# Performance work log

Hardware: AMD Instinct MI355X
Metric: run time of the kernel (lower is better)

## Reference

```python
import jax, jax.numpy as jnp
import numpy as np

N = 20000
NEG_SLOPE = 0.2


def gatv2_layer(x, src, dst, edge_attr, Wl, bl, Wr, br, We, att, bias, H, C):
    """PyG GATv2Conv: add self-loops (edge_attr fill='mean'), gather-score-softmax-aggregate."""
    n = x.shape[0]
    E = src.shape[0]
    # --- add self loops, self-loop edge_attr = mean of incoming edge_attr per node ---
    ea_sum = jax.ops.segment_sum(edge_attr, dst, num_segments=n)
    deg = jax.ops.segment_sum(jnp.ones((E, 1), x.dtype), dst, num_segments=n)
    ea_loop = ea_sum / jnp.maximum(deg, 1.0)
    loop = jnp.arange(n)
    src_a = jnp.concatenate([src, loop])
    dst_a = jnp.concatenate([dst, loop])
    ea = jnp.concatenate([edge_attr, ea_loop], axis=0)
    # --- linear projections ---
    xl = (x @ Wl + bl).reshape(n, H, C)   # source-side features
    xr = (x @ Wr + br).reshape(n, H, C)   # target-side features
    e = (ea @ We).reshape(-1, H, C)       # edge features
    # --- per-edge GATv2 attention score ---
    m = xl[src_a] + xr[dst_a] + e                          # [E', H, C]
    s = jnp.sum(jax.nn.leaky_relu(m, NEG_SLOPE) * att, -1)  # [E', H]
    # --- softmax over incoming edges of each target node ---
    smax = jax.ops.segment_max(s, dst_a, num_segments=n)
    ex = jnp.exp(s - smax[dst_a])
    denom = jax.ops.segment_sum(ex, dst_a, num_segments=n)
    alpha = ex / (denom[dst_a] + 1e-16)                    # [E', H]
    # --- aggregate messages (alpha * x_l[src]) ---
    out = jax.ops.segment_sum(alpha[..., None] * xl[src_a], dst_a, num_segments=n)
    return out.reshape(n, H * C) + bias


def setup_inputs() -> dict:
    key = jax.random.key(0)
    ks = jax.random.split(key, 20)
    F, HID, H1, A = 128, 32, 8, 128
    E = 640000
    d = {}
    d["x"] = jax.random.normal(ks[0], (N, F), jnp.float32)
    d["edge_index"] = jax.random.randint(ks[1], (2, E), 0, N, jnp.int32).astype(jnp.int64)
    d["edge_attr"] = jax.random.normal(ks[2], (E, 1), jnp.float32)
    # layer 1 params (in=F, out=HID, heads=H1)
    d["W1l"] = jax.random.normal(ks[3], (F, H1 * HID), jnp.float32) * 0.05
    d["b1l"] = jnp.zeros((H1 * HID,), jnp.float32)
    d["W1r"] = jax.random.normal(ks[4], (F, H1 * HID), jnp.float32) * 0.05
    d["b1r"] = jnp.zeros((H1 * HID,), jnp.float32)
    d["We1"] = jax.random.normal(ks[5], (1, H1 * HID), jnp.float32) * 0.05
    d["att1"] = jax.random.normal(ks[6], (H1, HID), jnp.float32) * 0.05
    d["bias1"] = jnp.zeros((H1 * HID,), jnp.float32)
    # layer 2 params (in=H1*HID, out=A, heads=1)
    d["W2l"] = jax.random.normal(ks[7], (H1 * HID, A), jnp.float32) * 0.05
    d["b2l"] = jnp.zeros((A,), jnp.float32)
    d["W2r"] = jax.random.normal(ks[8], (H1 * HID, A), jnp.float32) * 0.05
    d["b2r"] = jnp.zeros((A,), jnp.float32)
    d["We2"] = jax.random.normal(ks[9], (1, A), jnp.float32) * 0.05
    d["att2"] = jax.random.normal(ks[10], (1, A), jnp.float32) * 0.05
    d["bias2"] = jnp.zeros((A,), jnp.float32)
    d["alpha"] = jnp.array(0.0, jnp.float32)
    return d


def reference(x, edge_index, edge_attr, W1l, b1l, W1r, b1r, We1, att1, bias1,
              W2l, b2l, W2r, b2r, We2, att2, bias2, alpha):
    src, dst = edge_index[0], edge_index[1]
    h = jax.nn.relu(gatv2_layer(x, src, dst, edge_attr, W1l, b1l, W1r, b1r,
                                We1, att1, bias1, H=8, C=32))
    h = jax.nn.relu(gatv2_layer(h, src, dst, edge_attr, W2l, b2l, W2r, b2r,
                                We2, att2, bias2, H=1, C=128))
    pooled = jnp.mean(h, axis=0, keepdims=True)  # global_mean_pool, single graph -> [1, A]
    return jax.nn.softmax(pooled, axis=1), jax.nn.sigmoid(alpha)
```

## Files before the change

kernel.cpp:

```cpp
#include <hip/hip_runtime.h>
#include <math.h>

#define NEG_SLOPE 0.2f
#define LOG2E 1.4426950408889634f

typedef __attribute__((ext_vector_type(8))) short short8;
typedef __attribute__((ext_vector_type(4))) float f32x4;
typedef __attribute__((ext_vector_type(2))) float v2f;

__device__ __forceinline__ int imin(int a, int b) { return a < b ? a : b; }

__device__ __forceinline__ unsigned int f2bf(float f) {
    unsigned int u = __float_as_uint(f);
    return (u + 0x7fffu + ((u >> 16) & 1u)) >> 16;
}
__device__ __forceinline__ float fast_exp2(float x) {
#if __has_builtin(__builtin_amdgcn_exp2f)
    return __builtin_amdgcn_exp2f(x);
#else
    return exp2f(x);
#endif
}
__device__ __forceinline__ unsigned char f2fp8(float v) {
    return (unsigned char)(__builtin_amdgcn_cvt_pk_fp8_f32(v, v, 0, false) & 0xff);
}
template <int CTRL>
__device__ __forceinline__ float dpp_add(float v) {
    int t = __builtin_amdgcn_update_dpp(0, __float_as_int(v), CTRL, 0xF, 0xF, true);
    return v + __int_as_float(t);
}
__device__ __forceinline__ v2f pk_fma(v2f a, v2f b, v2f c) {
    v2f d;
    asm("v_pk_fma_f32 %0, %1, %2, %3" : "=v"(d) : "v"(a), "v"(b), "v"(c));
    return d;
}
__device__ __forceinline__ v2f pk_add(v2f a, v2f b) {
    v2f d;
    asm("v_pk_add_f32 %0, %1, %2" : "=v"(d) : "v"(a), "v"(b));
    return d;
}

__global__ void fused_prep(const int* __restrict__ ei, const float* __restrict__ ea,
                           unsigned long long* __restrict__ hist, int E,
                           const float* __restrict__ x, unsigned short* __restrict__ xb, int nF4,
                           const float* __restrict__ W1l, const float* __restrict__ W1r,
                           const float* __restrict__ W2l, const float* __restrict__ W2r,
                           const float* __restrict__ b1l, const float* __restrict__ b1r,
                           const float* __restrict__ b2l, const float* __restrict__ b2r,
                           unsigned short* __restrict__ Wt1, unsigned short* __restrict__ Wt2,
                           float* __restrict__ b1cat, float* __restrict__ b2cat,
                           int F, int HC1, int HC2) {
    int i = blockIdx.x * blockDim.x + threadIdx.x;
    if (i < E) {
        int d = ei[E + i];
        long long fx = (long long)__float2int_rn(ea[i] * 65536.0f);
        unsigned long long v = ((unsigned long long)fx << 32) | 1ull;
        atomicAdd(&hist[(size_t)d * 8], v);
        return;
    }
    int j = i - E;
    if (j < nF4) {
        float4 v = ((const float4*)x)[j];
        uint2 r;
        r.x = f2bf(v.x) | (f2bf(v.y) << 16);
        r.y = f2bf(v.z) | (f2bf(v.w) << 16);
        ((uint2*)xb)[j] = r;
        return;
    }
    int k = j - nF4;
    int S1 = F * HC1, S2 = HC1 * HC2;
    if (k < S1) {
        int kk = k / HC1, nn = k - kk * HC1;
        Wt1[(size_t)nn * F + kk] = (unsigned short)f2bf(W1l[k]);
    } else if (k < 2 * S1) {
        int m = k - S1;
        int kk = m / HC1, nn = m - kk * HC1;
        Wt1[(size_t)(HC1 + nn) * F + kk] = (unsigned short)f2bf(W1r[m]);
    } else if (k < 2 * S1 + S2) {
        int m = k - 2 * S1;
        int kk = m / HC2, nn = m - kk * HC2;
        Wt2[(size_t)nn * HC1 + kk] = (unsigned short)f2bf(W2l[m]);
    } else if (k < 2 * S1 + 2 * S2) {
        int m = k - 2 * S1 - S2;
        int kk = m / HC2, nn = m - kk * HC2;
        Wt2[(size_t)(HC2 + nn) * HC1 + kk] = (unsigned short)f2bf(W2r[m]);
    } else if (k < 2 * S1 + 2 * S2 + 2 * HC1) {
        int m = k - 2 * S1 - 2 * S2;
        b1cat[m] = (m < HC1) ? b1l[m] : b1r[m - HC1];
    } else if (k < 2 * S1 + 2 * S2 + 2 * HC1 + 2 * HC2) {
        int m = k - 2 * S1 - 2 * S2 - 2 * HC1;
        b2cat[m] = (m < HC2) ? b2l[m] : b2r[m - HC2];
    }
}

__global__ void scan_a(const unsigned long long* __restrict__ hist, int* __restrict__ bsum, int n) {
    __shared__ int wred[4];
    int base = blockIdx.x * 1024;
    int tid = threadIdx.x;
    int s = 0;
#pragma unroll
    for (int k = 0; k < 4; ++k) {
        int i = base + tid + k * 256;
        if (i < n) s += (int)(hist[(size_t)i * 8] & 0xffffffffull);
    }
#pragma unroll
    for (int off = 32; off > 0; off >>= 1) s += __shfl_xor(s, off, 64);
    if ((tid & 63) == 0) wred[tid >> 6] = s;
    __syncthreads();
    if (tid == 0) bsum[blockIdx.x] = wred[0] + wred[1] + wred[2] + wred[3];
}

__global__ void scan_c(const unsigned long long* __restrict__ hist,
                       const int* __restrict__ bsum, int* __restrict__ row_ptr,
                       int* __restrict__ wptr_pad, float* __restrict__ ea_loop,
                       int n, int B) {
    __shared__ int wtot[4];
    __shared__ int sh_base;
    int tid = threadIdx.x;
    int wid = tid >> 6, lane = tid & 63;
    int i0 = blockIdx.x * 1024 + tid * 4;
    int dcnt[4]; float esum[4];
#pragma unroll
    for (int k = 0; k < 4; ++k) {
        if (i0 + k < n) {
            unsigned long long h = hist[(size_t)(i0 + k) * 8];
            dcnt[k] = (int)(h & 0xffffffffull);
            esum[k] = (float)((int)(h >> 32)) * (1.0f / 65536.0f);
        } else { dcnt[k] = 0; esum[k] = 0.0f; }
    }
    int tsum = dcnt[0] + dcnt[1] + dcnt[2] + dcnt[3];
    int s = tsum;
#pragma unroll
    for (int off = 1; off < 64; off <<= 1) {
        int t = __shfl_up(s, off, 64);
        if (lane >= off) s += t;
    }
    if (lane == 63) wtot[wid] = s;
    if (tid < 64) {
        int v   = (tid < B) ? bsum[tid] : 0;
        int pre = (tid < (int)blockIdx.x) ? v : 0;
        int tot = v;
#pragma unroll
        for (int off = 32; off > 0; off >>= 1) {
            pre += __shfl_xor(pre, off, 64);
            tot += __shfl_xor(tot, off, 64);
        }
        if (tid == 0) {
            sh_base = pre;
            if (blockIdx.x == 0) row_ptr[n] = tot;
        }
    }
    __syncthreads();
    int wpre = 0;
#pragma unroll
    for (int k = 0; k < 4; ++k) if (k < wid) wpre += wtot[k];
    int pre = sh_base + wpre + (s - tsum);
    if (i0 < n) {
        int4 e;
        e.x = pre;
        e.y = pre + dcnt[0];
        e.z = e.y + dcnt[1];
        e.w = e.z + dcnt[2];
        *(int4*)(row_ptr + i0) = e;
        int ev[4] = { e.x, e.y, e.z, e.w };
        float4 el;
        el.x = esum[0] / fmaxf((float)dcnt[0], 1.0f);
        el.y = esum[1] / fmaxf((float)dcnt[1], 1.0f);
        el.z = esum[2] / fmaxf((float)dcnt[2], 1.0f);
        el.w = esum[3] / fmaxf((float)dcnt[3], 1.0f);
        *(float4*)(ea_loop + i0) = el;
#pragma unroll
        for (int k = 0; k < 4; ++k) wptr_pad[(size_t)(i0 + k) * 16] = ev[k];
    }
}

__global__ void edge_scatter(const int* __restrict__ ei, const float* __restrict__ ea,
                             int* __restrict__ wptr_pad, int2* __restrict__ spk, int E) {
    int e = blockIdx.x * blockDim.x + threadIdx.x;
    if (e < E) {
        int d = ei[E + e];
        int pos = atomicAdd(&wptr_pad[(size_t)d * 16], 1);
        spk[pos] = make_int2(ei[e], __float_as_int(ea[e]));
    }
}

template <bool OUT_FP8>
__global__ void __launch_bounds__(256)
gemm_bf16(const unsigned short* __restrict__ A, const unsigned short* __restrict__ Bt,
          const float* __restrict__ bias, void* __restrict__ Cv,
          int M, int N, int K) {
    __shared__ __attribute__((aligned(16))) unsigned short As[64 * 40];
    __shared__ __attribute__((aligned(16))) unsigned short Bs[64 * 40];
    int tid  = threadIdx.x;
    int wave = tid >> 6, lane = tid & 63;
    int m0 = blockIdx.x * 64, n0 = blockIdx.y * 64;
    int row = tid >> 2, kg = (tid & 3) * 8;

    f32x4 acc[4] = {};
    for (int kk = 0; kk < K; kk += 32) {
        int gm = m0 + row;
        uint4 av;
        if (gm < M) av = *(const uint4*)(A + (size_t)gm * K + kk + kg);
        else        av = make_uint4(0, 0, 0, 0);
        *(uint4*)&As[row * 40 + kg] = av;
        uint4 bv = *(const uint4*)(Bt + (size_t)(n0 + row) * K + kk + kg);
        *(uint4*)&Bs[row * 40 + kg] = bv;
        __syncthreads();
        short8 a = *(const short8*)&As[(wave * 16 + (lane & 15)) * 40 + (lane >> 4) * 8];
#pragma unroll
        for (int g = 0; g < 4; ++g) {
            short8 b = *(const short8*)&Bs[(g * 16 + (lane & 15)) * 40 + (lane >> 4) * 8];
            acc[g] = __builtin_amdgcn_mfma_f32_16x16x32_bf16(a, b, acc[g], 0, 0, 0);
        }
        __syncthreads();
    }
#pragma unroll
    for (int g = 0; g < 4; ++g) {
        int col = n0 + g * 16 + (lane & 15);
        float bs = bias[col];
#pragma unroll
        for (int r = 0; r < 4; ++r) {
            int grow = m0 + wave * 16 + (lane >> 4) * 4 + r;
            if (grow < M) {
                float val = acc[g][r] + bs;
                if constexpr (OUT_FP8) {
                    ((unsigned char*)Cv)[(size_t)grow * N + col] = f2fp8(val);
                } else {
                    ((unsigned short*)Cv)[(size_t)grow * N + col] = (unsigned short)f2bf(val);
                }
            }
        }
    }
}

template <int NG>
__device__ __forceinline__ void unp2(uint2 u, v2f* xf) {
    xf[0] = __builtin_amdgcn_cvt_pk_f32_fp8(u.x, false);
    xf[1] = __builtin_amdgcn_cvt_pk_f32_fp8(u.x, true);
    if constexpr (NG == 4) {
        xf[2] = __builtin_amdgcn_cvt_pk_f32_fp8(u.y, false);
        xf[3] = __builtin_amdgcn_cvt_pk_f32_fp8(u.y, true);
    }
}
template <int G>
__device__ __forceinline__ float grp_reduce32(float vs) {
    vs = dpp_add<0xB1>(vs);
    if constexpr (G >= 4)  vs = dpp_add<0x4E>(vs);
    if constexpr (G >= 8)  vs = dpp_add<0x141>(vs);
    if constexpr (G >= 16) vs = dpp_add<0x140>(vs);
    if constexpr (G >= 32) {
        int t = __builtin_amdgcn_ds_swizzle(__float_as_int(vs), 0x401F);
        vs += __int_as_float(t);
    }
    return vs;
}

template <int HC, int STRIDE, int C, int OUT_MODE>
__global__ void __launch_bounds__(256)
gat_agg(const unsigned char* __restrict__ xlr,
        const float* __restrict__ We, const float* __restrict__ att,
        const float* __restrict__ bias,
        const int* __restrict__ row_ptr, const int2* __restrict__ spk,
        const float* __restrict__ ea_loop,
        void* __restrict__ out, int n) {
    constexpr int NV = HC / 32;
    constexpr int NG = NV / 2;
    constexpr int G  = C / NV;
    constexpr int SHIFT = (STRIDE == 512) ? 9 : 8;
    constexpr float K23 = 2.0f / 3.0f;
    __shared__ float red[4][128];
    int wave = threadIdx.x >> 6;
    int lane = threadIdx.x & 63;
    int node = blockIdx.x * 4 + wave;
    bool active = node < n;
    if (OUT_MODE == 0 && !active) return;
    unsigned int lo32 = (unsigned int)(lane & 31) * NV;
    int half = lane >> 5;

    float vout[NV];
#pragma unroll
    for (int j = 0; j < NV; ++j) vout[j] = 0.0f;

    if (active) {
        auto ldd = [&](unsigned int off) -> uint2 {
            uint2 r;
            if constexpr (NV == 8) r = *(const uint2*)(xlr + off);
            else { r.x = *(const unsigned int*)(xlr + off); r.y = 0u; }
            return r;
        };
        auto gat = [&](int s) -> uint2 {
            return ldd(((unsigned int)s << SHIFT) + lo32);
        };

        v2f xr2[NG], We2[NG], att62[NG], o2[NG];
        unp2<NG>(ldd(((unsigned int)node << SHIFT) + HC + lo32), xr2);
#pragma unroll
        for (int g = 0; g < NG; ++g) {
            We2[g]   = *(const v2f*)(We  + lo32 + 2 * g);
            v2f a    = *(const v2f*)(att + lo32 + 2 * g);
            att62[g] = a * (0.6f * LOG2E);
            o2[g]    = v2f{0.0f, 0.0f};
        }
        float l = 0.0f;

        int start = __builtin_amdgcn_readfirstlane(row_ptr[node]);
        int end   = __builtin_amdgcn_readfirstlane(row_ptr[node + 1]);
        float ea_l = ea_loop[node];

        auto process = [&](uint2 du, float w, bool maskhi) {
            v2f xf[NG];
            unp2<NG>(du, xf);
            v2f w2 = {w, w};
            v2f vs6 = {0.0f, 0.0f};
            float vs4 = 0.0f;
#pragma unroll
            for (int g = 0; g < NG; ++g) {
                v2f t  = pk_fma(w2, We2[g], xr2[g]);
                v2f mm = pk_add(xf[g], t);
                vs6 = pk_fma(att62[g], mm, vs6);
                vs4 = fmaf(fabsf(mm.x), att62[g].x, vs4);
                vs4 = fmaf(fabsf(mm.y), att62[g].y, vs4);
            }
            float vs = fmaf(K23, vs4, vs6.x + vs6.y);
            vs = grp_reduce32<G>(vs);
            float pr = fast_exp2(vs);
            if (maskhi && lane >= 32) pr = 0.0f;
            l += pr;
            v2f pr2 = {pr, pr};
#pragma unroll
            for (int g = 0; g < NG; ++g) o2[g] = pk_fma(xf[g], pr2, o2[g]);
        };
        auto W = [&](int2 s) -> float { return __int_as_float(s.y); };

        process(ldd(((unsigned int)node << SHIFT) + lo32), ea_l, true);

        int cnt = end - start;
        int npair = cnt >> 1;
        const int2* pp = spk + start + half;

        if (npair >= 8) {
            int2 s0 = pp[0],  s1 = pp[2],  s2 = pp[4],  s3 = pp[6];
            int2 s4 = pp[8],  s5 = pp[10], s6 = pp[12], s7 = pp[14];
            uint2 g0 = gat(s0.x), g1 = gat(s1.x), g2 = gat(s2.x), g3 = gat(s3.x);
            int p = 0;
            for (; p + 16 <= npair; p += 8) {
                uint2 h0 = gat(s4.x), h1 = gat(s5.x), h2 = gat(s6.x), h3 = gat(s7.x);
                float w0 = W(s0), w1 = W(s1), w2 = W(s2), w3 = W(s3);
                s0 = pp[2*(p+8)];  s1 = pp[2*(p+9)];
                s2 = pp[2*(p+10)]; s3 = pp[2*(p+11)];
                process(g0, w0, false); process(g1, w1, false);
                process(g2, w2, false); process(g3, w3, false);
                g0 = gat(s0.x); g1 = gat(s1.x); g2 = gat(s2.x); g3 = gat(s3.x);
                float w4 = W(s4), w5 = W(s5), w6 = W(s6), w7 = W(s7);
                s4 = pp[2*(p+12)]; s5 = pp[2*(p+13)];
                s6 = pp[2*(p+14)]; s7 = pp[2*(p+15)];
                process(h0, w4, false); process(h1, w5, false);
                process(h2, w6, false); process(h3, w7, false);
            }
            uint2 h0 = gat(s4.x), h1 = gat(s5.x), h2 = gat(s6.x), h3 = gat(s7.x);
            process(g0, W(s0), false); process(g1, W(s1), false);
            process(g2, W(s2), false); process(g3, W(s3), false);
            process(h0, W(s4), false); process(h1, W(s5), false);
            process(h2, W(s6), false); process(h3, W(s7), false);
            for (int k = p + 8; k < npair; ++k) {
                int2 t = pp[2 * k];
                process(gat(t.x), W(t), false);
            }
        } else {
            for (int k = 0; k < npair; ++k) {
                int2 t = pp[2 * k];
                process(gat(t.x), W(t), false);
            }
        }
        if (cnt & 1) {
            int2 st = spk[end - 1];
            process(gat(st.x), W(st), true);
        }

        l += __shfl_xor(l, 32, 64);
#pragma unroll
        for (int g = 0; g < NG; ++g) {
            o2[g].x += __shfl_xor(o2[g].x, 32, 64);
            o2[g].y += __shfl_xor(o2[g].y, 32, 64);
        }
        float inv = 1.0f / (l + 1e-16f);

        if (lane < 32) {
#pragma unroll
            for (int g = 0; g < NG; ++g) {
                v2f b = *(const v2f*)(bias + lo32 + 2 * g);
                vout[2 * g]     = fmaxf(o2[g].x * inv + b.x, 0.0f);
                vout[2 * g + 1] = fmaxf(o2[g].y * inv + b.y, 0.0f);
            }
            if constexpr (OUT_MODE == 0) {
                unsigned short* op = (unsigned short*)out + (size_t)node * HC + lo32;
                if constexpr (NV == 8) {
                    uint4 t;
                    t.x = f2bf(vout[0]) | (f2bf(vout[1]) << 16);
                    t.y = f2bf(vout[2]) | (f2bf(vout[3]) << 16);
                    t.z = f2bf(vout[4]) | (f2bf(vout[5]) << 16);
                    t.w = f2bf(vout[6]) | (f2bf(vout[7]) << 16);
                    *(uint4*)op = t;
                } else {
                    uint2 t;
                    t.x = f2bf(vout[0]) | (f2bf(vout[1]) << 16);
                    t.y = f2bf(vout[2]) | (f2bf(vout[3]) << 16);
                    *(uint2*)op = t;
                }
            }
        }
    }

    if constexpr (OUT_MODE == 1) {
        if (lane < 32) {
#pragma unroll
            for (int j = 0; j < NV; ++j) red[wave][lo32 + j] = vout[j];
        }
        __syncthreads();
        if (wave == 0) {
            int c = lane;
            float a = red[0][c] + red[1][c] + red[2][c] + red[3][c];
            float b = red[0][c + 64] + red[1][c + 64] + red[2][c + 64] + red[3][c + 64];
            float* pacc = (float*)out + (size_t)(blockIdx.x & 255) * 128;
            atomicAdd(&pacc[c], a);
            atomicAdd(&pacc[c + 64], b);
        }
    }
}

__global__ void __launch_bounds__(1024)
pool_final(const float* __restrict__ partial, int nb,
           const float* __restrict__ alpha_in,
           float* __restrict__ out, int n) {
    __shared__ float acc[8][128];
    __shared__ float red[4];
    int t = threadIdx.x & 127;
    int g = threadIdx.x >> 7;
    float s = 0.0f;
    for (int b = g; b < nb; b += 8) s += partial[b * 128 + t];
    acc[g][t] = s;
    __syncthreads();
    if (threadIdx.x < 128) {
        float tot = 0.0f;
#pragma unroll
        for (int k = 0; k < 8; ++k) tot += acc[k][t];
        float mean = tot / (float)n;
        float mx = mean;
#pragma unroll
        for (int off = 32; off > 0; off >>= 1) mx = fmaxf(mx, __shfl_xor(mx, off, 64));
        if ((t & 63) == 0) red[t >> 6] = mx;
        __syncthreads();
        mx = fmaxf(red[0], red[1]);
        float ex = __expf(mean - mx);
        float sm = ex;
#pragma unroll
        for (int off = 32; off > 0; off >>= 1) sm += __shfl_xor(sm, off, 64);
        if ((t & 63) == 0) red[2 + (t >> 6)] = sm;
        __syncthreads();
        sm = red[2] + red[3];
        out[t] = ex / sm;
        if (t == 0) out[128] = 1.0f / (1.0f + __expf(-alpha_in[0]));
    }
}

extern "C" void kernel_launch(void* const* d_in, const int* in_sizes, int n_in,
                              void* d_out, int out_size, void* d_ws, size_t ws_size,
                              hipStream_t stream) {
    const float* x    = (const float*)d_in[0];
    const int*   ei   = (const int*)d_in[1];
    const float* ea   = (const float*)d_in[2];
    const float* W1l  = (const float*)d_in[3];
    const float* b1l  = (const float*)d_in[4];
    const float* W1r  = (const float*)d_in[5];
    const float* b1r  = (const float*)d_in[6];
    const float* We1  = (const float*)d_in[7];
    const float* att1 = (const float*)d_in[8];
    const float* bias1= (const float*)d_in[9];
    const float* W2l  = (const float*)d_in[10];
    const float* b2l  = (const float*)d_in[11];
    const float* W2r  = (const float*)d_in[12];
    const float* b2r  = (const float*)d_in[13];
    const float* We2  = (const float*)d_in[14];
    const float* att2 = (const float*)d_in[15];
    const float* bias2= (const float*)d_in[16];
    const float* alpha= (const float*)d_in[17];
    float* out = (float*)d_out;

    const int F = 128, HC1 = 256, HC2 = 128;
    const int n = in_sizes[0] / F;
    const int E = in_sizes[1] / 2;
    const int B = (n + 1023) / 1024;

    char* ws = (char*)d_ws;
    size_t off = 0;
    auto alloc = [&](size_t bytes) { size_t p = off; off += (bytes + 255) & ~(size_t)255; return p; };

    unsigned long long* hist = (unsigned long long*)(ws + alloc((size_t)n * 8 * 8));
    int*   row_ptr = (int*)  (ws + alloc((size_t)(n + 1) * 4));
    int*   wptr    = (int*)  (ws + alloc((size_t)n * 16 * 4));
    float* ea_loop = (float*)(ws + alloc((size_t)n * 4));
    int*   bsum    = (int*)  (ws + alloc(64 * 4));
    int2*  spk     = (int2*) (ws + alloc((size_t)E * 8));
    unsigned short* xb   = (unsigned short*)(ws + alloc((size_t)n * F * 2));
    unsigned short* Wt1  = (unsigned short*)(ws + alloc((size_t)F * (2 * HC1) * 2));
    unsigned short* Wt2  = (unsigned short*)(ws + alloc((size_t)HC1 * (2 * HC2) * 2));
    float* b1cat   = (float*)(ws + alloc((size_t)2 * HC1 * 4));
    float* b2cat   = (float*)(ws + alloc((size_t)2 * HC2 * 4));
    unsigned char* xlr1 = (unsigned char*)(ws + alloc((size_t)n * 2 * HC1));
    unsigned short* h1  = (unsigned short*)(ws + alloc((size_t)n * HC1 * 2));
    float* partial = (float*)(ws + alloc((size_t)256 * 128 * 4));
    unsigned char* xlr2 = xlr1;
    const int NB_SLOTS = 256;

    (void)hipMemsetAsync(hist, 0, (size_t)n * 8 * 8, stream);
    (void)hipMemsetAsync(partial, 0, (size_t)NB_SLOTS * 128 * 4, stream);

    int tb = 256;
    {
        int nF4  = n * F / 4;
        int WTOT = 2 * F * HC1 + 2 * HC1 * HC2 + 2 * HC1 + 2 * HC2;
        int total = E + nF4 + WTOT;
        fused_prep<<<(total + tb - 1) / tb, tb, 0, stream>>>(
            ei, ea, hist, E, x, xb, nF4,
            W1l, W1r, W2l, W2r, b1l, b1r, b2l, b2r,
            Wt1, Wt2, b1cat, b2cat, F, HC1, HC2);
    }
    scan_a<<<B, 256, 0, stream>>>(hist, bsum, n);
    scan_c<<<B, 256, 0, stream>>>(hist, bsum, row_ptr, wptr, ea_loop, n, B);
    edge_scatter<<<(E + tb - 1) / tb, tb, 0, stream>>>(ei, ea, wptr, spk, E);

    {
        dim3 grid((n + 63) / 64, (2 * HC1) / 64);
        gemm_bf16<true><<<grid, 256, 0, stream>>>(xb, Wt1, b1cat, xlr1, n, 2 * HC1, F);
    }
    gat_agg<256, 512, 32, 0><<<(n + 3) / 4, 256, 0, stream>>>(
        xlr1, We1, att1, bias1, row_ptr, spk, ea_loop, h1, n);

    {
        dim3 grid((n + 63) / 64, (2 * HC2) / 64);
        gemm_bf16<true><<<grid, 256, 0, stream>>>(h1, Wt2, b2cat, xlr2, n, 2 * HC2, HC1);
    }
    gat_agg<128, 256, 128, 1><<<(n + 3) / 4, 256, 0, stream>>>(
        xlr2, We2, att2, bias2, row_ptr, spk, ea_loop, partial, n);

    pool_final<<<1, 1024, 0, stream>>>(partial, NB_SLOTS, alpha, out, n);
}
```

Measured before the change: 279.1 us.

## Split each node's edge list across two waves and merge via shared memory

The GAT aggregation kernel now gives each destination node two waves instead of one. Each wave processes half of the edge pairs, and the partial softmax numerators and denominators are combined through shared memory behind a block barrier. The deep 8-way gather prefetch pipeline is replaced with a shallower 2-deep one. This doubles the grid and aims to raise memory-level parallelism per node, at the cost of an extra __syncthreads, shared-memory traffic and fewer loads in flight per wave.

New measurement: 273.9 us. About the same (-1.9%).

```diff
diff --git a/kernel.cpp b/kernel.cpp
--- a/kernel.cpp
+++ b/kernel.cpp
@@ -268,44 +268,49 @@
     constexpr int G  = C / NV;
     constexpr int SHIFT = (STRIDE == 512) ? 9 : 8;
     constexpr float K23 = 2.0f / 3.0f;
-    __shared__ float red[4][128];
+    __shared__ float lsh[2][32];
+    __shared__ float osh[2][HC];
+    __shared__ float red[2][128];
     int wave = threadIdx.x >> 6;
     int lane = threadIdx.x & 63;
-    int node = blockIdx.x * 4 + wave;
+    int nib  = wave >> 1;
+    int sub  = wave & 1;
+    int node = blockIdx.x * 2 + nib;
     bool active = node < n;
-    if (OUT_MODE == 0 && !active) return;
     unsigned int lo32 = (unsigned int)(lane & 31) * NV;
     int half = lane >> 5;
 
-    float vout[NV];
-#pragma unroll
-    for (int j = 0; j < NV; ++j) vout[j] = 0.0f;
+    v2f o2[NG];
+#pragma unroll
+    for (int g = 0; g < NG; ++g) o2[g] = v2f{0.0f, 0.0f};
+    float l = 0.0f;
+
+    v2f xr2[NG], We2[NG], att62[NG];
+
+    auto ldd = [&](unsigned int off) -> uint2 {
+        uint2 r;
+        if constexpr (NV == 8) r = *(const uint2*)(xlr + off);
+        else { r.x = *(const unsigned int*)(xlr + off); r.y = 0u; }
+        return r;
+    };
+    auto gat = [&](int s) -> uint2 {
+        return ldd(((unsigned int)s << SHIFT) + lo32);
+    };
+    auto W = [&](int2 s) -> float { return __int_as_float(s.y); };
 
     if (active) {
-        auto ldd = [&](unsigned int off) -> uint2 {
-            uint2 r;
-            if constexpr (NV == 8) r = *(const uint2*)(xlr + off);
-            else { r.x = *(const unsigned int*)(xlr + off); r.y = 0u; }
-            return r;
-        };
-        auto gat = [&](int s) -> uint2 {
-            return ldd(((unsigned int)s << SHIFT) + lo32);
-        };
-
-        v2f xr2[NG], We2[NG], att62[NG], o2[NG];
         unp2<NG>(ldd(((unsigned int)node << SHIFT) + HC + lo32), xr2);
 #pragma unroll
         for (int g = 0; g < NG; ++g) {
             We2[g]   = *(const v2f*)(We  + lo32 + 2 * g);
             v2f a    = *(const v2f*)(att + lo32 + 2 * g);
             att62[g] = a * (0.6f * LOG2E);
-            o2[g]    = v2f{0.0f, 0.0f};
-        }
-        float l = 0.0f;
+        }
 
         int start = __builtin_amdgcn_readfirstlane(row_ptr[node]);
         int end   = __builtin_amdgcn_readfirstlane(row_ptr[node + 1]);
-        float ea_l = ea_loop[node];
+        int cnt = end - start;
+        int npair = cnt >> 1;
 
         auto process = [&](uint2 du, float w, bool maskhi) {
             v2f xf[NG];
@@ -330,49 +335,41 @@
 #pragma unroll
             for (int g = 0; g < NG; ++g) o2[g] = pk_fma(xf[g], pr2, o2[g]);
         };
-        auto W = [&](int2 s) -> float { return __int_as_float(s.y); };
-
-        process(ldd(((unsigned int)node << SHIFT) + lo32), ea_l, true);
-
-        int cnt = end - start;
-        int npair = cnt >> 1;
-        const int2* pp = spk + start + half;
-
-        if (npair >= 8) {
-            int2 s0 = pp[0],  s1 = pp[2],  s2 = pp[4],  s3 = pp[6];
-            int2 s4 = pp[8],  s5 = pp[10], s6 = pp[12], s7 = pp[14];
-            uint2 g0 = gat(s0.x), g1 = gat(s1.x), g2 = gat(s2.x), g3 = gat(s3.x);
+
+        int lo = sub ? (npair >> 1) : 0;
+        int hi = sub ? npair : (npair >> 1);
+        int m = hi - lo;
+
+        if (sub == 0) {
+            float ea_l = ea_loop[node];
+            process(ldd(((unsigned int)node << SHIFT) + lo32), ea_l, true);
+        }
+
+        const int2* q = spk + start + half + 2 * lo;
+        if (m >= 2) {
+            int2 sA = q[0], sB = q[2];
+            uint2 gA = gat(sA.x);
             int p = 0;
-            for (; p + 16 <= npair; p += 8) {
-                uint2 h0 = gat(s4.x), h1 = gat(s5.x), h2 = gat(s6.x), h3 = gat(s7.x);
-                float w0 = W(s0), w1 = W(s1), w2 = W(s2), w3 = W(s3);
-                s0 = pp[2*(p+8)];  s1 = pp[2*(p+9)];
-                s2 = pp[2*(p+10)]; s3 = pp[2*(p+11)];
-                process(g0, w0, false); process(g1, w1, false);
-                process(g2, w2, false); process(g3, w3, false);
-                g0 = gat(s0.x); g1 = gat(s1.x); g2 = gat(s2.x); g3 = gat(s3.x);
-                float w4 = W(s4), w5 = W(s5), w6 = W(s6), w7 = W(s7);
-                s4 = pp[2*(p+12)]; s5 = pp[2*(p+13)];
-                s6 = pp[2*(p+14)]; s7 = pp[2*(p+15)];
-                process(h0, w4, false); process(h1, w5, false);
-                process(h2, w6, false); process(h3, w7, false);
+            for (; p + 4 <= m; p += 2) {
+                uint2 gB = gat(sB.x);
+                int2 sC = q[2 * (p + 2)], sD = q[2 * (p + 3)];
+                process(gA, W(sA), false);
+                uint2 gC = gat(sC.x);
+                process(gB, W(sB), false);
+                sA = sC; sB = sD; gA = gC;
             }
-            uint2 h0 = gat(s4.x), h1 = gat(s5.x), h2 = gat(s6.x), h3 = gat(s7.x);
-            process(g0, W(s0), false); process(g1, W(s1), false);
-            process(g2, W(s2), false); process(g3, W(s3), false);
-            process(h0, W(s4), false); process(h1, W(s5), false);
-            process(h2, W(s6), false); process(h3, W(s7), false);
-            for (int k = p + 8; k < npair; ++k) {
-                int2 t = pp[2 * k];
+            uint2 gB = gat(sB.x);
+            process(gA, W(sA), false);
+            process(gB, W(sB), false);
+            if (m - p == 3) {
+                int2 t = q[2 * (p + 2)];
                 process(gat(t.x), W(t), false);
             }
-        } else {
-            for (int k = 0; k < npair; ++k) {
-                int2 t = pp[2 * k];
-                process(gat(t.x), W(t), false);
-            }
-        }
-        if (cnt & 1) {
+        } else if (m == 1) {
+            int2 t = q[0];
+            process(gat(t.x), W(t), false);
+        }
+        if (sub == 1 && (cnt & 1)) {
             int2 st = spk[end - 1];
             process(gat(st.x), W(st), true);
         }
@@ -383,44 +380,61 @@
             o2[g].x += __shfl_xor(o2[g].x, 32, 64);
             o2[g].y += __shfl_xor(o2[g].y, 32, 64);
         }
+    }
+
+    if (sub == 1 && lane < 32) {
+        lsh[nib][lane] = l;
+#pragma unroll
+        for (int g = 0; g < NG; ++g) *(v2f*)&osh[nib][lo32 + 2 * g] = o2[g];
+    }
+    __syncthreads();
+
+    float vout[NV];
+#pragma unroll
+    for (int j = 0; j < NV; ++j) vout[j] = 0.0f;
+
+    if (sub == 0 && active && lane < 32) {
+        l += lsh[nib][lane];
+#pragma unroll
+        for (int g = 0; g < NG; ++g) {
+            v2f t = *(const v2f*)&osh[nib][lo32 + 2 * g];
+            o2[g] = pk_add(o2[g], t);
+        }
         float inv = 1.0f / (l + 1e-16f);
-
-        if (lane < 32) {
-#pragma unroll
-            for (int g = 0; g < NG; ++g) {
-                v2f b = *(const v2f*)(bias + lo32 + 2 * g);
-                vout[2 * g]     = fmaxf(o2[g].x * inv + b.x, 0.0f);
-                vout[2 * g + 1] = fmaxf(o2[g].y * inv + b.y, 0.0f);
+#pragma unroll
+        for (int g = 0; g < NG; ++g) {
+            v2f b = *(const v2f*)(bias + lo32 + 2 * g);
+            vout[2 * g]     = fmaxf(o2[g].x * inv + b.x, 0.0f);
+            vout[2 * g + 1] = fmaxf(o2[g].y * inv + b.y, 0.0f);
+        }
+        if constexpr (OUT_MODE == 0) {
+            unsigned short* op = (unsigned short*)out + (size_t)node * HC + lo32;
+            if constexpr (NV == 8) {
+                uint4 t;
+                t.x = f2bf(vout[0]) | (f2bf(vout[1]) << 16);
+                t.y = f2bf(vout[2]) | (f2bf(vout[3]) << 16);
+                t.z = f2bf(vout[4]) | (f2bf(vout[5]) << 16);
+                t.w = f2bf(vout[6]) | (f2bf(vout[7]) << 16);
+                *(uint4*)op = t;
+            } else {
+                uint2 t;
+                t.x = f2bf(vout[0]) | (f2bf(vout[1]) << 16);
+                t.y = f2bf(vout[2]) | (f2bf(vout[3]) << 16);
+                *(uint2*)op = t;
             }
-            if constexpr (OUT_MODE == 0) {
-                unsigned short* op = (unsigned short*)out + (size_t)node * HC + lo32;
-                if constexpr (NV == 8) {
-                    uint4 t;
-                    t.x = f2bf(vout[0]) | (f2bf(vout[1]) << 16);
-                    t.y = f2bf(vout[2]) | (f2bf(vout[3]) << 16);
-                    t.z = f2bf(vout[4]) | (f2bf(vout[5]) << 16);
-                    t.w = f2bf(vout[6]) | (f2bf(vout[7]) << 16);
-                    *(uint4*)op = t;
-                } else {
-                    uint2 t;
-                    t.x = f2bf(vout[0]) | (f2bf(vout[1]) << 16);
-                    t.y = f2bf(vout[2]) | (f2bf(vout[3]) << 16);
-                    *(uint2*)op = t;
-                }
-            }
         }
     }
 
     if constexpr (OUT_MODE == 1) {
-        if (lane < 32) {
-#pragma unroll
-            for (int j = 0; j < NV; ++j) red[wave][lo32 + j] = vout[j];
+        if (sub == 0 && lane < 32) {
+#pragma unroll
+            for (int j = 0; j < NV; ++j) red[nib][lo32 + j] = vout[j];
         }
         __syncthreads();
         if (wave == 0) {
             int c = lane;
-            float a = red[0][c] + red[1][c] + red[2][c] + red[3][c];
-            float b = red[0][c + 64] + red[1][c + 64] + red[2][c + 64] + red[3][c + 64];
+            float a = red[0][c] + red[1][c];
+            float b = red[0][c + 64] + red[1][c + 64];
             float* pacc = (float*)out + (size_t)(blockIdx.x & 255) * 128;
             atomicAdd(&pacc[c], a);
             atomicAdd(&pacc[c + 64], b);
@@ -533,14 +547,14 @@
         dim3 grid((n + 63) / 64, (2 * HC1) / 64);
         gemm_bf16<true><<<grid, 256, 0, stream>>>(xb, Wt1, b1cat, xlr1, n, 2 * HC1, F);
     }
-    gat_agg<256, 512, 32, 0><<<(n + 3) / 4, 256, 0, stream>>>(
+    gat_agg<256, 512, 32, 0><<<(n + 1) / 2, 256, 0, stream>>>(
         xlr1, We1, att1, bias1, row_ptr, spk, ea_loop, h1, n);
 
     {
         dim3 grid((n + 63) / 64, (2 * HC2) / 64);
         gemm_bf16<true><<<grid, 256, 0, stream>>>(h1, Wt2, b2cat, xlr2, n, 2 * HC2, HC1);
     }
-    gat_agg<128, 256, 128, 1><<<(n + 3) / 4, 256, 0, stream>>>(
+    gat_agg<128, 256, 128, 1><<<(n + 1) / 2, 256, 0, stream>>>(
         xlr2, We2, att2, bias2, row_ptr, spk, ea_loop, partial, n);
 
     pool_final<<<1, 1024, 0, stream>>>(partial, NB_SLOTS, alpha, out, n);
```
